# Optimization experiments

Measured on AMD Instinct MI355X. Metric: run time of the kernel, lower is better.

The kernel has to match this reference:

```python
import jax, jax.numpy as jnp
import numpy as np

B, MENU, N, M = 4096, 256, 8, 16


def setup_inputs() -> dict:
    key = jax.random.key(0)
    k1, k2, k3, k4 = jax.random.split(key, 4)
    input_bids = jax.random.uniform(k1, (B, N, M), dtype=jnp.float32)
    allocs = jax.random.uniform(k2, (B, MENU, N, M), dtype=jnp.float32)
    # bidder weights must be strictly positive (divided by in payments)
    w = jax.random.uniform(k3, (B, N), dtype=jnp.float32, minval=0.5, maxval=1.5)
    b = jax.random.normal(k4, (B, MENU), dtype=jnp.float32)
    softmax_temp = jnp.asarray(100.0, dtype=jnp.float32)
    return {"input_bids": input_bids, "allocs": allocs, "w": w, "b": b,
            "softmax_temp": softmax_temp}


def reference(input_bids, allocs, w, b, softmax_temp):
    Bsz, n, m = input_bids.shape
    # append the "null" menu entry (zero allocation, zero boost)
    allocs = jnp.concatenate([allocs, jnp.zeros((Bsz, 1, n, m), allocs.dtype)], axis=1)  # B,S,n,m
    b = jnp.concatenate([b, jnp.zeros((Bsz, 1), b.dtype)], axis=1)                        # B,S

    # utility of each agent under each menu entry
    util = jnp.einsum('bsnm,bnm->bsn', allocs, input_bids)        # B,S,n
    per_agent_welfare = w[:, None, :] * util                      # B,S,n
    total_welfare = per_agent_welfare.sum(-1)                     # B,S

    alloc_choice = jax.nn.softmax((total_welfare + b) * softmax_temp, axis=-1)  # B,S
    item_allocation = jnp.einsum('bs,bsnm->bnm', alloc_choice, allocs)          # B,n,m
    chosen_welfare = jnp.einsum('bsn,bs->bn', per_agent_welfare, alloc_choice)  # B,n

    # leave-one-out (VCG-style) payments, vectorized over the removed agent i
    mask = 1.0 - jnp.eye(n, dtype=per_agent_welfare.dtype)        # n,n; row i zeros agent i
    removed_welfare = per_agent_welfare[None] * mask[:, None, None, :]  # i,B,S,n
    total_removed = removed_welfare.sum(-1)                       # i,B,S
    removed_choice = jax.nn.softmax((total_removed + b[None]) * softmax_temp, axis=-1)  # i,B,S

    removed_chosen_sum = jnp.einsum('ibsn,ibs->ib', removed_welfare, removed_choice)  # i,B
    masked_chosen_sum = jnp.einsum('bn,in->ib', chosen_welfare, mask)                 # i,B
    removed_b = jnp.einsum('ibs,bs->ib', removed_choice, b)                           # i,B
    alloc_b = jnp.einsum('bs,bs->b', alloc_choice, b)                                 # B

    payments = (removed_chosen_sum + removed_b - masked_chosen_sum - alloc_b[None]) / w.T  # n,B
    return alloc_choice, item_allocation, payments, allocs
```

## Files before the change

### kernel.cpp

```cpp
#include <hip/hip_runtime.h>

#define NAGENTS 8
#define NM 128
#define MENU 256
#define SFULL 257

#define BAR() asm volatile("s_waitcnt lgkmcnt(0)\n\ts_barrier" ::: "memory")

__device__ __forceinline__ float wredmax(float v) {
#pragma unroll
    for (int o = 32; o; o >>= 1) v = fmaxf(v, __shfl_xor(v, o));
    return v;
}
__device__ __forceinline__ float wredsum(float v) {
#pragma unroll
    for (int o = 32; o; o >>= 1) v += __shfl_xor(v, o);
    return v;
}

__global__ __launch_bounds__(1024, 4) void cama_kernel(
    const float* __restrict__ bids,
    const float* __restrict__ allocs,
    const float* __restrict__ wvec,
    const float* __restrict__ bvec,
    const float* __restrict__ tempp,
    float* __restrict__ out, int Bsz, int iters)
{
    __shared__ float4 lda4[MENU * 32];
    __shared__ float lds_pwT[NAGENTS * MENU];
    __shared__ float lds_tot[MENU];
    __shared__ float lds_bb[2][MENU];
    __shared__ __align__(16) float lds_bids[2][NM];
    __shared__ float lds_w[2][NAGENTS];
    __shared__ float lds_ch[SFULL];
    __shared__ float lds_rcs[NAGENTS], lds_rb[NAGENTS], lds_cw[NAGENTS];
    __shared__ float lds_ab;

    const int u = threadIdx.x;
    const int lane = u & 63;
    const int wave = u >> 6;
    const int n = u & 7;
    const int sg = u >> 3;

    float* out_choice = out;
    float* out_item   = out + (size_t)Bsz * SFULL;
    float* out_pay    = out_item + (size_t)Bsz * NM;
    float* out_all    = out_pay + (size_t)NAGENTS * Bsz;

    const float temp = tempp[0];

    size_t a = (size_t)blockIdx.x * iters;

    float Pf[2][16];

    {
        float rbb = 0.f, rbid = 0.f, rw = 0.f;
        if (u < MENU)    rbb  = bvec[a * MENU + u];
        if (u < NM)      rbid = bids[a * NM + u];
        if (u < NAGENTS) rw   = wvec[a * NAGENTS + u];
        const float4* s0 = (const float4*)(allocs + (a * MENU + sg) * NM) + (n << 2);
        const float4* s1 = (const float4*)(allocs + (a * MENU + 128 + sg) * NM) + (n << 2);
        float4 a0 = s0[0], a1 = s0[1], a2 = s0[2], a3 = s0[3];
        float4 b0 = s1[0], b1 = s1[1], b2 = s1[2], b3 = s1[3];
        Pf[0][0]=a0.x;  Pf[0][1]=a0.y;  Pf[0][2]=a0.z;  Pf[0][3]=a0.w;
        Pf[0][4]=a1.x;  Pf[0][5]=a1.y;  Pf[0][6]=a1.z;  Pf[0][7]=a1.w;
        Pf[0][8]=a2.x;  Pf[0][9]=a2.y;  Pf[0][10]=a2.z; Pf[0][11]=a2.w;
        Pf[0][12]=a3.x; Pf[0][13]=a3.y; Pf[0][14]=a3.z; Pf[0][15]=a3.w;
        Pf[1][0]=b0.x;  Pf[1][1]=b0.y;  Pf[1][2]=b0.z;  Pf[1][3]=b0.w;
        Pf[1][4]=b1.x;  Pf[1][5]=b1.y;  Pf[1][6]=b1.z;  Pf[1][7]=b1.w;
        Pf[1][8]=b2.x;  Pf[1][9]=b2.y;  Pf[1][10]=b2.z; Pf[1][11]=b2.w;
        Pf[1][12]=b3.x; Pf[1][13]=b3.y; Pf[1][14]=b3.z; Pf[1][15]=b3.w;
        if (u < MENU)    lds_bb[0][u]   = rbb;
        if (u < NM)      lds_bids[0][u] = rbid;
        if (u < NAGENTS) lds_w[0][u]    = rw;
    }
    BAR();

    for (int it = 0; it < iters; ++it) {
        const int p = it & 1;

        float qf[16];
        {
            const float4* bq = (const float4*)(&lds_bids[p][0]) + (n << 2);
            float4 qa = bq[0], qb = bq[1], qc = bq[2], qd = bq[3];
            qf[0]=qa.x; qf[1]=qa.y; qf[2]=qa.z; qf[3]=qa.w;
            qf[4]=qb.x; qf[5]=qb.y; qf[6]=qb.z; qf[7]=qb.w;
            qf[8]=qc.x; qf[9]=qc.y; qf[10]=qc.z; qf[11]=qc.w;
            qf[12]=qd.x; qf[13]=qd.y; qf[14]=qd.z; qf[15]=qd.w;
        }
        const float w_n = lds_w[p][n];
#pragma unroll
        for (int c = 0; c < 2; ++c) {
            const int s = (c << 7) + sg;
            float4 v0 = make_float4(Pf[c][0],  Pf[c][1],  Pf[c][2],  Pf[c][3]);
            float4 v1 = make_float4(Pf[c][4],  Pf[c][5],  Pf[c][6],  Pf[c][7]);
            float4 v2 = make_float4(Pf[c][8],  Pf[c][9],  Pf[c][10], Pf[c][11]);
            float4 v3 = make_float4(Pf[c][12], Pf[c][13], Pf[c][14], Pf[c][15]);
            float4* dst = (float4*)(out_all + (a * SFULL + s) * NM) + (n << 2);
            dst[0] = v0; dst[1] = v1; dst[2] = v2; dst[3] = v3;
            float util = 0.f;
#pragma unroll
            for (int k = 0; k < 16; ++k) util += Pf[c][k] * qf[k];
            float pwv = w_n * util;
            lds_pwT[(n << 8) + (s ^ (n << 2))] = pwv;
            float t4 = pwv;
            t4 += __shfl_xor(t4, 1);
            t4 += __shfl_xor(t4, 2);
            t4 += __shfl_xor(t4, 4);
            if (n == 0) lds_tot[s] = t4;
            const int base = s << 5, c7 = s & 7, j0 = n << 2;
            lda4[base + ((j0 + 0) ^ c7)] = v0;
            lda4[base + ((j0 + 1) ^ c7)] = v1;
            lda4[base + ((j0 + 2) ^ c7)] = v2;
            lda4[base + ((j0 + 3) ^ c7)] = v3;
        }
        if (u < 32)
            ((float4*)(out_all + (a * SFULL + MENU) * NM))[u] =
                make_float4(0.f, 0.f, 0.f, 0.f);

        const bool has_next = (it + 1 < iters);
        const size_t an = a + 1;
        float rbb2 = 0.f, rbid2 = 0.f, rw2 = 0.f;
        if (has_next) {
            if (u < MENU)    rbb2  = bvec[an * MENU + u];
            if (u < NM)      rbid2 = bids[an * NM + u];
            if (u < NAGENTS) rw2   = wvec[an * NAGENTS + u];
            const float4* s0 = (const float4*)(allocs + (an * MENU + sg) * NM) + (n << 2);
            const float4* s1 = (const float4*)(allocs + (an * MENU + 128 + sg) * NM) + (n << 2);
            float4 a0 = s0[0], a1 = s0[1], a2 = s0[2], a3 = s0[3];
            float4 b0 = s1[0], b1 = s1[1], b2 = s1[2], b3 = s1[3];
            Pf[0][0]=a0.x;  Pf[0][1]=a0.y;  Pf[0][2]=a0.z;  Pf[0][3]=a0.w;
            Pf[0][4]=a1.x;  Pf[0][5]=a1.y;  Pf[0][6]=a1.z;  Pf[0][7]=a1.w;
            Pf[0][8]=a2.x;  Pf[0][9]=a2.y;  Pf[0][10]=a2.z; Pf[0][11]=a2.w;
            Pf[0][12]=a3.x; Pf[0][13]=a3.y; Pf[0][14]=a3.z; Pf[0][15]=a3.w;
            Pf[1][0]=b0.x;  Pf[1][1]=b0.y;  Pf[1][2]=b0.z;  Pf[1][3]=b0.w;
            Pf[1][4]=b1.x;  Pf[1][5]=b1.y;  Pf[1][6]=b1.z;  Pf[1][7]=b1.w;
            Pf[1][8]=b2.x;  Pf[1][9]=b2.y;  Pf[1][10]=b2.z; Pf[1][11]=b2.w;
            Pf[1][12]=b3.x; Pf[1][13]=b3.y; Pf[1][14]=b3.z; Pf[1][15]=b3.w;
        }
        BAR();

        if (wave == 0) {
            float xs[4], bl[4], es[4];
            float mx = -1e30f;
#pragma unroll
            for (int c = 0; c < 4; ++c) {
                int v = (c << 6) | lane;
                bl[c] = lds_bb[p][v];
                float x = (lds_tot[v] + bl[c]) * temp;
                xs[c] = x; mx = fmaxf(mx, x);
            }
            mx = fmaxf(wredmax(mx), 0.f);
            float se = 0.f, sab = 0.f;
#pragma unroll
            for (int c = 0; c < 4; ++c) { es[c] = __expf(xs[c] - mx); se += es[c]; sab += es[c] * bl[c]; }
            float en = __expf(-mx);
            se = wredsum(se) + en;
            sab = wredsum(sab);
            float inv = 1.f / se;
#pragma unroll
            for (int c = 0; c < 4; ++c) {
                int v = (c << 6) | lane;
                float chv = es[c] * inv;
                lds_ch[v] = chv;
                out_choice[a * SFULL + v] = chv;
            }
            if (lane == 0) {
                float chn = en * inv;
                lds_ch[MENU] = chn;
                out_choice[a * SFULL + MENU] = chn;
                lds_ab = sab * inv;
            }
        } else if (wave <= 8) {
            const int i = wave - 1;
            float xs[4], trs[4], bl[4];
            float mx = -1e30f;
#pragma unroll
            for (int c = 0; c < 4; ++c) {
                int v = (c << 6) | lane;
                bl[c] = lds_bb[p][v];
                float tr = lds_tot[v] - lds_pwT[(i << 8) + (v ^ (i << 2))];
                trs[c] = tr;
                float x = (tr + bl[c]) * temp;
                xs[c] = x; mx = fmaxf(mx, x);
            }
            mx = fmaxf(wredmax(mx), 0.f);
            float se = 0.f, s1 = 0.f, s2 = 0.f;
#pragma unroll
            for (int c = 0; c < 4; ++c) {
                float e = __expf(xs[c] - mx);
                se += e; s1 += e * trs[c]; s2 += e * bl[c];
            }
            se = wredsum(se) + __expf(-mx);
            s1 = wredsum(s1);
            s2 = wredsum(s2);
            if (lane == 0) { lds_rcs[i] = s1 / se; lds_rb[i] = s2 / se; }
        }
        BAR();

        if (wave < 8) {
            const int i = wave;
            float cwv = 0.f;
#pragma unroll
            for (int c = 0; c < 4; ++c) {
                int v = (c << 6) | lane;
                cwv += lds_ch[v] * lds_pwT[(i << 8) + (v ^ (i << 2))];
            }
            cwv = wredsum(cwv);
            if (lane == 0) lds_cw[i] = cwv;
        }
        {
            const float* ldf = (const float*)lda4;
            const int wl = lane & 7, chunk = lane >> 3;
            const int nm = (wave << 3) + wl;
            const int jj = nm >> 2, r = nm & 3;
            float acc = 0.f;
#pragma unroll 8
            for (int it2 = 0; it2 < 32; ++it2) {
                int s = (it2 << 3) + chunk;
                acc += lds_ch[s] * ldf[(((s << 5) + (jj ^ (s & 7))) << 2) + r];
            }
            acc += __shfl_xor(acc, 8);
            acc += __shfl_xor(acc, 16);
            acc += __shfl_xor(acc, 32);
            if (chunk == 0) out_item[a * NM + nm] = acc;
        }
        if (has_next) {
            if (u < MENU)    lds_bb[p ^ 1][u]   = rbb2;
            if (u < NM)      lds_bids[p ^ 1][u] = rbid2;
            if (u < NAGENTS) lds_w[p ^ 1][u]    = rw2;
        }
        BAR();

        if (u < NAGENTS) {
            float ctot = 0.f;
#pragma unroll
            for (int k = 0; k < NAGENTS; ++k) ctot += lds_cw[k];
            float pay = (lds_rcs[u] + lds_rb[u] - (ctot - lds_cw[u]) - lds_ab)
                        / lds_w[p][u];
            out_pay[(size_t)u * Bsz + a] = pay;
        }
        a = an;
    }
}

extern "C" void kernel_launch(void* const* d_in, const int* in_sizes, int n_in,
                              void* d_out, int out_size, void* d_ws, size_t ws_size,
                              hipStream_t stream) {
    const float* bids   = (const float*)d_in[0];
    const float* allocs = (const float*)d_in[1];
    const float* wvec   = (const float*)d_in[2];
    const float* bvec   = (const float*)d_in[3];
    const float* tempp  = (const float*)d_in[4];
    float* out = (float*)d_out;
    const int Bsz = in_sizes[0] / NM;
    const int nblocks = 256;
    const int iters = Bsz / nblocks;
    cama_kernel<<<nblocks, 1024, 0, stream>>>(bids, allocs, wvec, bvec, tempp,
                                              out, Bsz, iters);
}
```

Measured before the change: 267.9 us.

## Remap threads to contiguous float4s and compute item allocation from registers

```diff
diff --git a/kernel.cpp b/kernel.cpp
--- a/kernel.cpp
+++ b/kernel.cpp
@@ -26,50 +26,43 @@
     const float* __restrict__ tempp,
     float* __restrict__ out, int Bsz, int iters)
 {
-    __shared__ float4 lda4[MENU * 32];
     __shared__ float lds_pwT[NAGENTS * MENU];
     __shared__ float lds_tot[MENU];
     __shared__ float lds_bb[2][MENU];
     __shared__ __align__(16) float lds_bids[2][NM];
     __shared__ float lds_w[2][NAGENTS];
     __shared__ float lds_ch[SFULL];
+    __shared__ __align__(16) float lds_scr[16 * NM];
     __shared__ float lds_rcs[NAGENTS], lds_rb[NAGENTS], lds_cw[NAGENTS];
     __shared__ float lds_ab;
 
     const int u = threadIdx.x;
     const int lane = u & 63;
     const int wave = u >> 6;
-    const int n = u & 7;
-    const int sg = u >> 3;
+    const int n  = (u >> 2) & 7;
+    const int mq = u & 3;
+    const int su = u >> 5;
 
     float* out_choice = out;
     float* out_item   = out + (size_t)Bsz * SFULL;
     float* out_pay    = out_item + (size_t)Bsz * NM;
     float* out_all    = out_pay + (size_t)NAGENTS * Bsz;
+    float4* out_all4  = (float4*)out_all;
+    const float4* all4 = (const float4*)allocs;
 
     const float temp = tempp[0];
-
     size_t a = (size_t)blockIdx.x * iters;
 
-    float Pf[2][16];
+    float4 Pf[8];
 
     {
         float rbb = 0.f, rbid = 0.f, rw = 0.f;
         if (u < MENU)    rbb  = bvec[a * MENU + u];
         if (u < NM)      rbid = bids[a * NM + u];
         if (u < NAGENTS) rw   = wvec[a * NAGENTS + u];
-        const float4* s0 = (const float4*)(allocs + (a * MENU + sg) * NM) + (n << 2);
-        const float4* s1 = (const float4*)(allocs + (a * MENU + 128 + sg) * NM) + (n << 2);
-        float4 a0 = s0[0], a1 = s0[1], a2 = s0[2], a3 = s0[3];
-        float4 b0 = s1[0], b1 = s1[1], b2 = s1[2], b3 = s1[3];
-        Pf[0][0]=a0.x;  Pf[0][1]=a0.y;  Pf[0][2]=a0.z;  Pf[0][3]=a0.w;
-        Pf[0][4]=a1.x;  Pf[0][5]=a1.y;  Pf[0][6]=a1.z;  Pf[0][7]=a1.w;
-        Pf[0][8]=a2.x;  Pf[0][9]=a2.y;  Pf[0][10]=a2.z; Pf[0][11]=a2.w;
-        Pf[0][12]=a3.x; Pf[0][13]=a3.y; Pf[0][14]=a3.z; Pf[0][15]=a3.w;
-        Pf[1][0]=b0.x;  Pf[1][1]=b0.y;  Pf[1][2]=b0.z;  Pf[1][3]=b0.w;
-        Pf[1][4]=b1.x;  Pf[1][5]=b1.y;  Pf[1][6]=b1.z;  Pf[1][7]=b1.w;
-        Pf[1][8]=b2.x;  Pf[1][9]=b2.y;  Pf[1][10]=b2.z; Pf[1][11]=b2.w;
-        Pf[1][12]=b3.x; Pf[1][13]=b3.y; Pf[1][14]=b3.z; Pf[1][15]=b3.w;
+#pragma unroll
+        for (int k = 0; k < 8; ++k)
+            Pf[k] = all4[a * 8192 + (k << 10) + u];
         if (u < MENU)    lds_bb[0][u]   = rbb;
         if (u < NM)      lds_bids[0][u] = rbid;
         if (u < NAGENTS) lds_w[0][u]    = rw;
@@ -78,65 +71,44 @@
 
     for (int it = 0; it < iters; ++it) {
         const int p = it & 1;
-
-        float qf[16];
-        {
-            const float4* bq = (const float4*)(&lds_bids[p][0]) + (n << 2);
-            float4 qa = bq[0], qb = bq[1], qc = bq[2], qd = bq[3];
-            qf[0]=qa.x; qf[1]=qa.y; qf[2]=qa.z; qf[3]=qa.w;
-            qf[4]=qb.x; qf[5]=qb.y; qf[6]=qb.z; qf[7]=qb.w;
-            qf[8]=qc.x; qf[9]=qc.y; qf[10]=qc.z; qf[11]=qc.w;
-            qf[12]=qd.x; qf[13]=qd.y; qf[14]=qd.z; qf[15]=qd.w;
-        }
-        const float w_n = lds_w[p][n];
-#pragma unroll
-        for (int c = 0; c < 2; ++c) {
-            const int s = (c << 7) + sg;
-            float4 v0 = make_float4(Pf[c][0],  Pf[c][1],  Pf[c][2],  Pf[c][3]);
-            float4 v1 = make_float4(Pf[c][4],  Pf[c][5],  Pf[c][6],  Pf[c][7]);
-            float4 v2 = make_float4(Pf[c][8],  Pf[c][9],  Pf[c][10], Pf[c][11]);
-            float4 v3 = make_float4(Pf[c][12], Pf[c][13], Pf[c][14], Pf[c][15]);
-            float4* dst = (float4*)(out_all + (a * SFULL + s) * NM) + (n << 2);
-            dst[0] = v0; dst[1] = v1; dst[2] = v2; dst[3] = v3;
-            float util = 0.f;
-#pragma unroll
-            for (int k = 0; k < 16; ++k) util += Pf[c][k] * qf[k];
-            float pwv = w_n * util;
-            lds_pwT[(n << 8) + (s ^ (n << 2))] = pwv;
-            float t4 = pwv;
-            t4 += __shfl_xor(t4, 1);
-            t4 += __shfl_xor(t4, 2);
-            t4 += __shfl_xor(t4, 4);
-            if (n == 0) lds_tot[s] = t4;
-            const int base = s << 5, c7 = s & 7, j0 = n << 2;
-            lda4[base + ((j0 + 0) ^ c7)] = v0;
-            lda4[base + ((j0 + 1) ^ c7)] = v1;
-            lda4[base + ((j0 + 2) ^ c7)] = v2;
-            lda4[base + ((j0 + 3) ^ c7)] = v3;
-        }
-        if (u < 32)
-            ((float4*)(out_all + (a * SFULL + MENU) * NM))[u] =
-                make_float4(0.f, 0.f, 0.f, 0.f);
-
         const bool has_next = (it + 1 < iters);
         const size_t an = a + 1;
+
+        float4 Sf[8];
+#pragma unroll
+        for (int k = 0; k < 8; ++k) Sf[k] = Pf[k];
+
         float rbb2 = 0.f, rbid2 = 0.f, rw2 = 0.f;
         if (has_next) {
+#pragma unroll
+            for (int k = 0; k < 8; ++k)
+                Pf[k] = all4[an * 8192 + (k << 10) + u];
             if (u < MENU)    rbb2  = bvec[an * MENU + u];
             if (u < NM)      rbid2 = bids[an * NM + u];
             if (u < NAGENTS) rw2   = wvec[an * NAGENTS + u];
-            const float4* s0 = (const float4*)(allocs + (an * MENU + sg) * NM) + (n << 2);
-            const float4* s1 = (const float4*)(allocs + (an * MENU + 128 + sg) * NM) + (n << 2);
-            float4 a0 = s0[0], a1 = s0[1], a2 = s0[2], a3 = s0[3];
-            float4 b0 = s1[0], b1 = s1[1], b2 = s1[2], b3 = s1[3];
-            Pf[0][0]=a0.x;  Pf[0][1]=a0.y;  Pf[0][2]=a0.z;  Pf[0][3]=a0.w;
-            Pf[0][4]=a1.x;  Pf[0][5]=a1.y;  Pf[0][6]=a1.z;  Pf[0][7]=a1.w;
-            Pf[0][8]=a2.x;  Pf[0][9]=a2.y;  Pf[0][10]=a2.z; Pf[0][11]=a2.w;
-            Pf[0][12]=a3.x; Pf[0][13]=a3.y; Pf[0][14]=a3.z; Pf[0][15]=a3.w;
-            Pf[1][0]=b0.x;  Pf[1][1]=b0.y;  Pf[1][2]=b0.z;  Pf[1][3]=b0.w;
-            Pf[1][4]=b1.x;  Pf[1][5]=b1.y;  Pf[1][6]=b1.z;  Pf[1][7]=b1.w;
-            Pf[1][8]=b2.x;  Pf[1][9]=b2.y;  Pf[1][10]=b2.z; Pf[1][11]=b2.w;
-            Pf[1][12]=b3.x; Pf[1][13]=b3.y; Pf[1][14]=b3.z; Pf[1][15]=b3.w;
+        }
+
+#pragma unroll
+        for (int k = 0; k < 8; ++k)
+            out_all4[a * 8224 + (k << 10) + u] = Sf[k];
+        if (u < 32)
+            out_all4[a * 8224 + 8192 + u] = make_float4(0.f, 0.f, 0.f, 0.f);
+
+        const float4 q4 = ((const float4*)&lds_bids[p][0])[u & 31];
+        const float w_n = lds_w[p][n];
+#pragma unroll
+        for (int k = 0; k < 8; ++k) {
+            const int s = (k << 5) + su;
+            float util = Sf[k].x*q4.x + Sf[k].y*q4.y + Sf[k].z*q4.z + Sf[k].w*q4.w;
+            util += __shfl_xor(util, 1);
+            util += __shfl_xor(util, 2);
+            float pwv = w_n * util;
+            if (mq == 0) lds_pwT[(n << 8) + (s ^ (n << 2))] = pwv;
+            float t = pwv;
+            t += __shfl_xor(t, 4);
+            t += __shfl_xor(t, 8);
+            t += __shfl_xor(t, 16);
+            if ((lane & 31) == 0) lds_tot[s] = t;
         }
         BAR();
 
@@ -210,20 +182,19 @@
             if (lane == 0) lds_cw[i] = cwv;
         }
         {
-            const float* ldf = (const float*)lda4;
-            const int wl = lane & 7, chunk = lane >> 3;
-            const int nm = (wave << 3) + wl;
-            const int jj = nm >> 2, r = nm & 3;
-            float acc = 0.f;
-#pragma unroll 8
-            for (int it2 = 0; it2 < 32; ++it2) {
-                int s = (it2 << 3) + chunk;
-                acc += lds_ch[s] * ldf[(((s << 5) + (jj ^ (s & 7))) << 2) + r];
-            }
-            acc += __shfl_xor(acc, 8);
-            acc += __shfl_xor(acc, 16);
-            acc += __shfl_xor(acc, 32);
-            if (chunk == 0) out_item[a * NM + nm] = acc;
+            float ax = 0.f, ay = 0.f, az = 0.f, aw = 0.f;
+#pragma unroll
+            for (int k = 0; k < 8; ++k) {
+                float chv = lds_ch[(k << 5) + su];
+                ax += Sf[k].x * chv; ay += Sf[k].y * chv;
+                az += Sf[k].z * chv; aw += Sf[k].w * chv;
+            }
+            ax += __shfl_xor(ax, 32);
+            ay += __shfl_xor(ay, 32);
+            az += __shfl_xor(az, 32);
+            aw += __shfl_xor(aw, 32);
+            if (lane < 32)
+                ((float4*)lds_scr)[(wave << 5) + lane] = make_float4(ax, ay, az, aw);
         }
         if (has_next) {
             if (u < MENU)    lds_bb[p ^ 1][u]   = rbb2;
@@ -232,6 +203,12 @@
         }
         BAR();
 
+        if (u < NM) {
+            float s = 0.f;
+#pragma unroll
+            for (int w = 0; w < 16; ++w) s += lds_scr[(w << 7) + u];
+            out_item[a * NM + u] = s;
+        }
         if (u < NAGENTS) {
             float ctot = 0.f;
 #pragma unroll
```

New measurement: 242.6 us. -9.4%, faster.
